# Kernel optimization log

Hardware: AMD Instinct MI355X
Metric: run time of the kernel (lower is better)

## Reference

```python
import jax, jax.numpy as jnp
import numpy as np
import math

B, S, D, H = 2, 2048, 1024, 16
DK = D // H


def setup_inputs() -> dict:
    key = jax.random.key(0)
    ks = jax.random.split(key, 12)
    s = 1.0 / math.sqrt(D)
    inp = {
        "query": jax.random.normal(ks[0], (B, S, D), jnp.float32),
        "key": jax.random.normal(ks[1], (B, S, D), jnp.float32),
        "value": jax.random.normal(ks[2], (B, S, D), jnp.float32),
        # causal mask, 0 = masked
        "mask": jnp.tril(jnp.ones((S, S), jnp.int32))[None].repeat(B, axis=0),
        "Wq": jax.random.normal(ks[3], (D, D), jnp.float32) * s,
        "bq": jnp.zeros((D,), jnp.float32),
        "Wk": jax.random.normal(ks[4], (D, D), jnp.float32) * s,
        "bk": jnp.zeros((D,), jnp.float32),
        "Wv": jax.random.normal(ks[5], (D, D), jnp.float32) * s,
        "bv": jnp.zeros((D,), jnp.float32),
        "Wo": jax.random.normal(ks[6], (D, D), jnp.float32) * s,
        "bo": jnp.zeros((D,), jnp.float32),
    }
    return inp


def _split_heads(x):
    # [B, S, D] -> [B, H, S, DK]
    b, s, _ = x.shape
    return x.reshape(b, s, H, DK).transpose(0, 2, 1, 3)


def reference(query, key, value, mask, Wq, bq, Wk, bk, Wv, bv, Wo, bo):
    q = _split_heads(query @ Wq + bq)
    k = _split_heads(key @ Wk + bk)
    v = _split_heads(value @ Wv + bv)
    scores = jnp.einsum("bhqd,bhkd->bhqk", q, k) / math.sqrt(DK)
    # mask: [B, Sq, Sk] -> broadcast over heads; 0 entries get -1e9
    scores = jnp.where(mask[:, None, :, :] == 0, jnp.float32(-1e9), scores)
    p = jax.nn.softmax(scores, axis=-1)  # dropout p=0 (eval) -> identity
    x = jnp.einsum("bhqk,bhkd->bhqd", p, v)
    x = x.transpose(0, 2, 1, 3).reshape(query.shape[0], -1, D)
    return x @ Wo + bo
```

## Files before the change

### kernel.cpp

```cpp
#include <hip/hip_runtime.h>
#include <hip/hip_bf16.h>
#include <stdint.h>


constexpr int BATCH = 2, SEQ = 2048, DIM = 1024, NH = 16, HD = 64;
constexpr int MROWS = BATCH * SEQ;

typedef __attribute__((ext_vector_type(4))) float f32x4;
typedef __attribute__((ext_vector_type(8))) short bf16x8;
typedef __attribute__((ext_vector_type(4))) int i32x4;

#define DEVI __device__ __forceinline__

DEVI ushort f2bf(float f) {
  __hip_bfloat16 h = __float2bfloat16(f);
  return __builtin_bit_cast(ushort, h);
}

DEVI f32x4 mfma16(bf16x8 a, bf16x8 b, f32x4 c) {
  return __builtin_amdgcn_mfma_f32_16x16x32_bf16(a, b, c, 0, 0, 0);
}

#if __has_builtin(__builtin_amdgcn_exp2f)
DEVI float fexp2(float x) { return __builtin_amdgcn_exp2f(x); }
#else
DEVI float fexp2(float x) { return exp2f(x); }
#endif

DEVI void gload16(const ushort* g, ushort* l) {
  __builtin_amdgcn_global_load_lds((const __attribute__((address_space(1))) void*)g,
                                   (__attribute__((address_space(3))) void*)l,
                                   16, 0, 0);
}

DEVI i32x4 cvt8(f32x4 a, f32x4 b) {
  union { ushort u[8]; i32x4 v; } r;
  #pragma unroll
  for (int j = 0; j < 4; ++j) r.u[j] = f2bf(a[j]);
  #pragma unroll
  for (int j = 0; j < 4; ++j) r.u[4 + j] = f2bf(b[j]);
  return r.v;
}

__global__ __launch_bounds__(256) void tw(const float* __restrict__ w0,
                                          const float* __restrict__ w1,
                                          const float* __restrict__ w2,
                                          const float* __restrict__ w3,
                                          ushort* __restrict__ t0,
                                          ushort* __restrict__ t1,
                                          ushort* __restrict__ t2,
                                          ushort* __restrict__ t3) {
  const float* W = blockIdx.z == 0 ? w0 : blockIdx.z == 1 ? w1 : blockIdx.z == 2 ? w2 : w3;
  ushort* T = blockIdx.z == 0 ? t0 : blockIdx.z == 1 ? t1 : blockIdx.z == 2 ? t2 : t3;
  __shared__ float tile[32][33];
  int k0 = blockIdx.x * 32, n0 = blockIdx.y * 32;
  int tx = threadIdx.x & 31, ty = threadIdx.x >> 5;
  #pragma unroll
  for (int i = 0; i < 32; i += 8) tile[ty + i][tx] = W[(size_t)(k0 + ty + i) * DIM + n0 + tx];
  __syncthreads();
  #pragma unroll
  for (int i = 0; i < 32; i += 8) T[(size_t)(n0 + ty + i) * DIM + k0 + tx] = f2bf(tile[tx][ty + i]);
}

struct GemmPtrs {
  const void* A[3];
  const ushort* Bt[3];
  const float* bias[3];
  void* C[3];
  float scale[3];
};

template <bool F32OUT, bool VT, bool AF32>
__global__ __launch_bounds__(256, 3) void gemm_bt(GemmPtrs gp, int M, int N, int K) {
  const int z = blockIdx.z;
  const float* __restrict__ A32 = (const float*)gp.A[z];
  const ushort* __restrict__ A16 = (const ushort*)gp.A[z];
  const ushort* __restrict__ Bt = gp.Bt[z];
  const float* __restrict__ bias = gp.bias[z];
  const float scale = gp.scale[z];
  const bool vsw = VT && (z == 2);

  __shared__ __align__(16) ushort As[2][128 * 32];
  __shared__ __align__(16) ushort Bs[2][128 * 32];

  const int tid = threadIdx.x;
  const int lane = tid & 63, wv = tid >> 6;
  const int wm = wv >> 1, wn = wv & 1;
  const int l15 = lane & 15, lg = lane >> 4;

  const int flat = blockIdx.y * 8 + blockIdx.x;
  const int xcd = flat & 7;
  const int j = flat >> 3;
  const int mslice = (int)gridDim.y >> 3;
  const int mpan = xcd * mslice + (j >> 3);
  const int npan = j & 7;
  const int m0 = mpan * 128, n0 = npan * 128;

  f32x4 acc[4][4];
  #pragma unroll
  for (int i = 0; i < 4; ++i)
    #pragma unroll
    for (int j2 = 0; j2 < 4; ++j2) acc[i][j2] = f32x4{0.f, 0.f, 0.f, 0.f};

  const int ci0 = tid, ci1 = tid + 256;
  const int ar0 = m0 + (ci0 >> 2), ar1 = m0 + (ci1 >> 2);
  const int ak0 = (ci0 & 3) * 8, ak1 = (ci1 & 3) * 8;
  const ushort* Ab0 = A16 + (size_t)ar0 * K + ak0;
  const ushort* Ab1 = A16 + (size_t)ar1 * K + ak1;
  const float* Af0 = A32 + (size_t)ar0 * K + ak0;
  const float* Af1 = A32 + (size_t)ar1 * K + ak1;
  const ushort* Bb0 = Bt + (size_t)(n0 + (ci0 >> 2)) * K + ak0;
  const ushort* Bb1 = Bt + (size_t)(n0 + (ci1 >> 2)) * K + ak1;

  f32x4 sA0, sA1, sA2, sA3;

  const int nk = K >> 5;
  if (AF32) {
    sA0 = *(const f32x4*)(Af0);     sA1 = *(const f32x4*)(Af0 + 4);
    sA2 = *(const f32x4*)(Af1);     sA3 = *(const f32x4*)(Af1 + 4);
    *(i32x4*)&As[0][ci0 * 8] = cvt8(sA0, sA1);
    *(i32x4*)&As[0][ci1 * 8] = cvt8(sA2, sA3);
    gload16(Bb0, &Bs[0][ci0 * 8]);
    gload16(Bb1, &Bs[0][ci1 * 8]);
    sA0 = *(const f32x4*)(Af0 + 32); sA1 = *(const f32x4*)(Af0 + 36);
    sA2 = *(const f32x4*)(Af1 + 32); sA3 = *(const f32x4*)(Af1 + 36);
  } else {
    gload16(Ab0, &As[0][ci0 * 8]);
    gload16(Ab1, &As[0][ci1 * 8]);
    gload16(Bb0, &Bs[0][ci0 * 8]);
    gload16(Bb1, &Bs[0][ci1 * 8]);
  }

  for (int kt = 0; kt < nk; ++kt) {
    const int cur = kt & 1;
    if (kt + 1 < nk) {
      const int ko = (kt + 1) << 5;
      if (!AF32) {
        gload16(Ab0 + ko, &As[cur ^ 1][ci0 * 8]);
        gload16(Ab1 + ko, &As[cur ^ 1][ci1 * 8]);
      }
      gload16(Bb0 + ko, &Bs[cur ^ 1][ci0 * 8]);
      gload16(Bb1 + ko, &Bs[cur ^ 1][ci1 * 8]);
      if (AF32)
        asm volatile("s_waitcnt vmcnt(6)" ::: "memory");
      else
        asm volatile("s_waitcnt vmcnt(4)" ::: "memory");
    } else {
      asm volatile("s_waitcnt vmcnt(0)" ::: "memory");
    }
    __builtin_amdgcn_s_barrier();
    __builtin_amdgcn_sched_barrier(0);

    const ushort* Afr = vsw ? &Bs[cur][0] : &As[cur][0];
    const ushort* Bfr = vsw ? &As[cur][0] : &Bs[cur][0];
    bf16x8 af[4], bfr[4];
    #pragma unroll
    for (int i = 0; i < 4; ++i) af[i] = *(const bf16x8*)&Afr[(wm * 64 + i * 16 + l15) * 32 + lg * 8];
    #pragma unroll
    for (int i = 0; i < 4; ++i) bfr[i] = *(const bf16x8*)&Bfr[(wn * 64 + i * 16 + l15) * 32 + lg * 8];
    #pragma unroll
    for (int i = 0; i < 4; ++i)
      #pragma unroll
      for (int j2 = 0; j2 < 4; ++j2) acc[i][j2] = mfma16(af[i], bfr[j2], acc[i][j2]);

    if (AF32 && kt + 1 < nk) {
      *(i32x4*)&As[cur ^ 1][ci0 * 8] = cvt8(sA0, sA1);
      *(i32x4*)&As[cur ^ 1][ci1 * 8] = cvt8(sA2, sA3);
      if (kt + 2 < nk) {
        const int ko2 = (kt + 2) << 5;
        sA0 = *(const f32x4*)(Af0 + ko2); sA1 = *(const f32x4*)(Af0 + ko2 + 4);
        sA2 = *(const f32x4*)(Af1 + ko2); sA3 = *(const f32x4*)(Af1 + ko2 + 4);
      }
      __builtin_amdgcn_sched_barrier(0);
      asm volatile("s_waitcnt lgkmcnt(0)" ::: "memory");
    }
    __builtin_amdgcn_s_barrier();
  }

  if (vsw) {
    ushort* Vt = (ushort*)gp.C[z];
    #pragma unroll
    for (int i = 0; i < 4; ++i)
      #pragma unroll
      for (int r = 0; r < 4; ++r) {
        int ch = n0 + wm * 64 + i * 16 + lg * 4 + r;
        float bch = bias[ch];
        int hh = ch >> 6, dch = ch & 63;
        #pragma unroll
        for (int j2 = 0; j2 < 4; ++j2) {
          int tok = m0 + wn * 64 + j2 * 16 + l15;
          int bb = tok >> 11, s = tok & 2047;
          float val = (acc[i][j2][r] + bch) * scale;
          Vt[(((size_t)bb * 16 + hh) * 64 + dch) * 2048 + s] = f2bf(val);
        }
      }
  } else {
    float bv[4];
    #pragma unroll
    for (int j2 = 0; j2 < 4; ++j2) bv[j2] = bias[n0 + wn * 64 + j2 * 16 + l15];
    #pragma unroll
    for (int i = 0; i < 4; ++i)
      #pragma unroll
      for (int j2 = 0; j2 < 4; ++j2)
        #pragma unroll
        for (int r = 0; r < 4; ++r) {
          int row = m0 + wm * 64 + i * 16 + lg * 4 + r;
          int col = n0 + wn * 64 + j2 * 16 + l15;
          float val = (acc[i][j2][r] + bv[j2]) * scale;
          if (F32OUT)
            ((float*)gp.C[z])[(size_t)row * N + col] = val;
          else
            ((ushort*)gp.C[z])[(size_t)row * N + col] = f2bf(val);
        }
  }
}

__global__ __launch_bounds__(256, 3) void attn(const ushort* __restrict__ Qp,
                                               const ushort* __restrict__ Kp,
                                               const ushort* __restrict__ Vtg,
                                               ushort* __restrict__ Xb) {
  __shared__ __align__(16) ushort Kl[2][64 * 64];
  __shared__ __align__(16) ushort Vl[2][64 * 64];
  __shared__ __align__(16) ushort Pl[4][16 * 64];

  const int bh = blockIdx.x;
  const int qt = (int)gridDim.y - 1 - (int)blockIdx.y;
  const int b = bh >> 4, h = bh & 15;
  const int tid = threadIdx.x;
  const int wv = tid >> 6, lane = tid & 63;
  const int l15 = lane & 15, lg = lane >> 4;
  const int swz = (l15 & 7) << 4;

  const size_t base = ((size_t)b * SEQ) * DIM + (size_t)h * HD;
  const ushort* Vtb = Vtg + (size_t)bh * HD * SEQ;

  const int qrow = qt * 64 + wv * 16 + l15;

  const ushort* qp = Qp + base + (size_t)qrow * DIM + lg * 8;
  bf16x8 qa[2] = {*(const bf16x8*)qp, *(const bf16x8*)(qp + 32)};

  f32x4 o[4];
  #pragma unroll
  for (int i = 0; i < 4; ++i) o[i] = f32x4{0.f, 0.f, 0.f, 0.f};
  float l_run = 0.f;

  const int ntiles = qt + 1;

  const int srow0 = tid >> 3, sc8 = tid & 7;
  const int srow1 = srow0 + 32;
  const int soff0 = (srow0 * 128 + sc8 * 16) ^ ((srow0 & 7) << 4);
  const int soff1 = (srow1 * 128 + sc8 * 16) ^ ((srow1 & 7) << 4);
  const ushort* Kb = Kp + base;

  i32x4 rk0 = *(const i32x4*)(Kb + (size_t)srow0 * DIM + sc8 * 8);
  i32x4 rk1 = *(const i32x4*)(Kb + (size_t)srow1 * DIM + sc8 * 8);
  i32x4 rv0 = *(const i32x4*)(Vtb + (size_t)srow0 * SEQ + sc8 * 8);
  i32x4 rv1 = *(const i32x4*)(Vtb + (size_t)srow1 * SEQ + sc8 * 8);
  *(i32x4*)((char*)&Kl[0][0] + soff0) = rk0;
  *(i32x4*)((char*)&Kl[0][0] + soff1) = rk1;
  *(i32x4*)((char*)&Vl[0][0] + soff0) = rv0;
  *(i32x4*)((char*)&Vl[0][0] + soff1) = rv1;

  for (int t = 0; t < ntiles; ++t) {
    const int cur = t & 1;
    const int kv0 = t * 64;

    if (t + 1 < ntiles) {
      const ushort* Kn = Kb + (size_t)(kv0 + 64) * DIM;
      const ushort* Vn = Vtb + (size_t)(kv0 + 64);
      rk0 = *(const i32x4*)(Kn + (size_t)srow0 * DIM + sc8 * 8);
      rk1 = *(const i32x4*)(Kn + (size_t)srow1 * DIM + sc8 * 8);
      rv0 = *(const i32x4*)(Vn + (size_t)srow0 * SEQ + sc8 * 8);
      rv1 = *(const i32x4*)(Vn + (size_t)srow1 * SEQ + sc8 * 8);
    }
    __syncthreads();

    const char* KL = (const char*)&Kl[cur][0];
    const char* VL = (const char*)&Vl[cur][0];

    f32x4 sc[4];
    #pragma unroll
    for (int n = 0; n < 4; ++n) sc[n] = f32x4{0.f, 0.f, 0.f, 0.f};
    __builtin_amdgcn_s_setprio(1);
    #pragma unroll
    for (int n = 0; n < 4; ++n) {
      #pragma unroll
      for (int kc = 0; kc < 2; ++kc) {
        int off = ((16 * n + l15) * 128 + kc * 64 + lg * 16) ^ swz;
        bf16x8 kf = *(const bf16x8*)(KL + off);
        sc[n] = mfma16(kf, qa[kc], sc[n]);
      }
    }
    __builtin_amdgcn_s_setprio(0);

    if (t == ntiles - 1) {
      #pragma unroll
      for (int n = 0; n < 4; ++n) {
        int kb0 = kv0 + 16 * n + lg * 4;
        #pragma unroll
        for (int r = 0; r < 4; ++r)
          if (kb0 + r > qrow) sc[n][r] = -1e30f;
      }
    }

    float rsum = 0.f;
    #pragma unroll
    for (int n = 0; n < 4; ++n)
      #pragma unroll
      for (int r = 0; r < 4; ++r) {
        float p = fexp2(sc[n][r]);
        sc[n][r] = p;
        rsum += p;
      }
    l_run += rsum;

    ushort* pb = &Pl[wv][0];
    #pragma unroll
    for (int n = 0; n < 4; ++n) {
      ushort4 pk = {f2bf(sc[n][0]), f2bf(sc[n][1]), f2bf(sc[n][2]), f2bf(sc[n][3])};
      int off = (l15 * 128 + n * 32 + lg * 8) ^ swz;
      *(ushort4*)((char*)pb + off) = pk;
    }
    bf16x8 pa[2];
    #pragma unroll
    for (int kc = 0; kc < 2; ++kc) {
      int off = (l15 * 128 + kc * 64 + lg * 16) ^ swz;
      pa[kc] = *(const bf16x8*)((char*)pb + off);
    }

    __builtin_amdgcn_s_setprio(1);
    #pragma unroll
    for (int kc = 0; kc < 2; ++kc)
      #pragma unroll
      for (int nd = 0; nd < 4; ++nd) {
        int off = ((16 * nd + l15) * 128 + kc * 64 + lg * 16) ^ swz;
        bf16x8 vf = *(const bf16x8*)(VL + off);
        o[nd] = mfma16(vf, pa[kc], o[nd]);
      }
    __builtin_amdgcn_s_setprio(0);

    if (t + 1 < ntiles) {
      char* KLn = (char*)&Kl[cur ^ 1][0];
      char* VLn = (char*)&Vl[cur ^ 1][0];
      *(i32x4*)(KLn + soff0) = rk0;
      *(i32x4*)(KLn + soff1) = rk1;
      *(i32x4*)(VLn + soff0) = rv0;
      *(i32x4*)(VLn + soff1) = rv1;
    }
  }

  float s = l_run;
  s += __shfl_xor(s, 16);
  s += __shfl_xor(s, 32);
  const float inv = 1.0f / s;
  ushort* xp = Xb + base + (size_t)qrow * DIM;
  #pragma unroll
  for (int nd = 0; nd < 4; ++nd) {
    ushort4 xk = {f2bf(o[nd][0] * inv), f2bf(o[nd][1] * inv),
                  f2bf(o[nd][2] * inv), f2bf(o[nd][3] * inv)};
    *(ushort4*)(xp + nd * 16 + lg * 4) = xk;
  }
}

extern "C" void kernel_launch(void* const* d_in, const int* in_sizes, int n_in,
                              void* d_out, int out_size, void* d_ws, size_t ws_size,
                              hipStream_t stream) {
  const float* query = (const float*)d_in[0];
  const float* keyp  = (const float*)d_in[1];
  const float* value = (const float*)d_in[2];
  const float* Wq = (const float*)d_in[4];
  const float* bq = (const float*)d_in[5];
  const float* Wk = (const float*)d_in[6];
  const float* bk = (const float*)d_in[7];
  const float* Wv = (const float*)d_in[8];
  const float* bv = (const float*)d_in[9];
  const float* Wo = (const float*)d_in[10];
  const float* bo = (const float*)d_in[11];
  float* out = (float*)d_out;

  char* w = (char*)d_ws;
  const size_t MAT = (size_t)MROWS * DIM * sizeof(ushort);
  const size_t WMT = (size_t)DIM * DIM * sizeof(ushort);
  ushort* WqT = (ushort*)w; w += WMT;
  ushort* WkT = (ushort*)w; w += WMT;
  ushort* WvT = (ushort*)w; w += WMT;
  ushort* WoT = (ushort*)w; w += WMT;
  ushort* Qp  = (ushort*)w; w += MAT;
  ushort* Kp  = (ushort*)w; w += MAT;
  ushort* Vt  = (ushort*)w; w += MAT;
  ushort* Xb  = (ushort*)w; w += MAT;

  tw<<<dim3(32, 32, 4), 256, 0, stream>>>(Wq, Wk, Wv, Wo, WqT, WkT, WvT, WoT);

  GemmPtrs g1;
  g1.A[0] = query; g1.A[1] = keyp; g1.A[2] = value;
  g1.Bt[0] = WqT; g1.Bt[1] = WkT; g1.Bt[2] = WvT;
  g1.bias[0] = bq; g1.bias[1] = bk; g1.bias[2] = bv;
  g1.C[0] = Qp; g1.C[1] = Kp; g1.C[2] = Vt;
  g1.scale[0] = 0.125f * 1.4426950408889634f; g1.scale[1] = 1.f; g1.scale[2] = 1.f;
  gemm_bt<false, true, true><<<dim3(DIM / 128, MROWS / 128, 3), 256, 0, stream>>>(g1, MROWS, DIM, DIM);

  attn<<<dim3(BATCH * NH, SEQ / 64), 256, 0, stream>>>(Qp, Kp, Vt, Xb);

  GemmPtrs g2;
  g2.A[0] = Xb; g2.A[1] = Xb; g2.A[2] = Xb;
  g2.Bt[0] = WoT; g2.Bt[1] = WoT; g2.Bt[2] = WoT;
  g2.bias[0] = bo; g2.bias[1] = bo; g2.bias[2] = bo;
  g2.C[0] = out; g2.C[1] = out; g2.C[2] = out;
  g2.scale[0] = 1.f; g2.scale[1] = 1.f; g2.scale[2] = 1.f;
  gemm_bt<true, false, false><<<dim3(DIM / 128, MROWS / 128, 1), 256, 0, stream>>>(g2, MROWS, DIM, DIM);
}
```

Baseline: 104.2 us.

## Stage fp32 A tiles directly to LDS with swizzle, convert to bf16 at fragment load

```diff
diff --git a/kernel.cpp b/kernel.cpp
--- a/kernel.cpp
+++ b/kernel.cpp
@@ -27,14 +27,14 @@
 DEVI float fexp2(float x) { return exp2f(x); }
 #endif
 
-DEVI void gload16(const ushort* g, ushort* l) {
+DEVI void gload16(const void* g, void* l) {
   __builtin_amdgcn_global_load_lds((const __attribute__((address_space(1))) void*)g,
                                    (__attribute__((address_space(3))) void*)l,
                                    16, 0, 0);
 }
 
-DEVI i32x4 cvt8(f32x4 a, f32x4 b) {
-  union { ushort u[8]; i32x4 v; } r;
+DEVI bf16x8 cvt8bf(f32x4 a, f32x4 b) {
+  union { ushort u[8]; bf16x8 v; } r;
   #pragma unroll
   for (int j = 0; j < 4; ++j) r.u[j] = f2bf(a[j]);
   #pragma unroll
@@ -70,7 +70,7 @@
   float scale[3];
 };
 
-template <bool F32OUT, bool VT, bool AF32>
+template <bool F32OUT, bool VT, bool AF32L>
 __global__ __launch_bounds__(256, 3) void gemm_bt(GemmPtrs gp, int M, int N, int K) {
   const int z = blockIdx.z;
   const float* __restrict__ A32 = (const float*)gp.A[z];
@@ -80,8 +80,9 @@
   const float scale = gp.scale[z];
   const bool vsw = VT && (z == 2);
 
-  __shared__ __align__(16) ushort As[2][128 * 32];
-  __shared__ __align__(16) ushort Bs[2][128 * 32];
+  constexpr int ASZ = AF32L ? 16384 : 8192;
+  __shared__ __align__(16) char As[2][ASZ];
+  __shared__ __align__(16) char Bs[2][8192];
 
   const int tid = threadIdx.x;
   const int lane = tid & 63, wv = tid >> 6;
@@ -103,45 +104,54 @@
     for (int j2 = 0; j2 < 4; ++j2) acc[i][j2] = f32x4{0.f, 0.f, 0.f, 0.f};
 
   const int ci0 = tid, ci1 = tid + 256;
-  const int ar0 = m0 + (ci0 >> 2), ar1 = m0 + (ci1 >> 2);
-  const int ak0 = (ci0 & 3) * 8, ak1 = (ci1 & 3) * 8;
-  const ushort* Ab0 = A16 + (size_t)ar0 * K + ak0;
-  const ushort* Ab1 = A16 + (size_t)ar1 * K + ak1;
-  const float* Af0 = A32 + (size_t)ar0 * K + ak0;
-  const float* Af1 = A32 + (size_t)ar1 * K + ak1;
-  const ushort* Bb0 = Bt + (size_t)(n0 + (ci0 >> 2)) * K + ak0;
-  const ushort* Bb1 = Bt + (size_t)(n0 + (ci1 >> 2)) * K + ak1;
-
-  f32x4 sA0, sA1, sA2, sA3;
+  const ushort* Bb0 = Bt + (size_t)(n0 + (ci0 >> 2)) * K + (ci0 & 3) * 8;
+  const ushort* Bb1 = Bt + (size_t)(n0 + (ci1 >> 2)) * K + (ci1 & 3) * 8;
+
+  const float* Af0s; const float* Af1s; const float* Af2s; const float* Af3s;
+  const ushort* Ab0; const ushort* Ab1;
+  int D0, D1, D2, D3;
+  if (AF32L) {
+    D0 = (tid + 0) * 16;   D1 = (tid + 256) * 16;
+    D2 = (tid + 512) * 16; D3 = (tid + 768) * 16;
+    int L0 = D0 ^ (((D0 >> 7) & 7) << 4);
+    int L1 = D1 ^ (((D1 >> 7) & 7) << 4);
+    int L2 = D2 ^ (((D2 >> 7) & 7) << 4);
+    int L3 = D3 ^ (((D3 >> 7) & 7) << 4);
+    Af0s = A32 + (size_t)(m0 + (L0 >> 7)) * K + ((L0 & 127) >> 2);
+    Af1s = A32 + (size_t)(m0 + (L1 >> 7)) * K + ((L1 & 127) >> 2);
+    Af2s = A32 + (size_t)(m0 + (L2 >> 7)) * K + ((L2 & 127) >> 2);
+    Af3s = A32 + (size_t)(m0 + (L3 >> 7)) * K + ((L3 & 127) >> 2);
+    Ab0 = nullptr; Ab1 = nullptr;
+  } else {
+    Ab0 = A16 + (size_t)(m0 + (ci0 >> 2)) * K + (ci0 & 3) * 8;
+    Ab1 = A16 + (size_t)(m0 + (ci1 >> 2)) * K + (ci1 & 3) * 8;
+    Af0s = Af1s = Af2s = Af3s = nullptr;
+    D0 = ci0 * 16; D1 = ci1 * 16; D2 = D3 = 0;
+  }
+
+  auto STAGE = [&](int buf, int kt) {
+    const int kof = kt << 5;
+    if (AF32L) {
+      gload16(Af0s + kof, &As[buf][D0]);
+      gload16(Af1s + kof, &As[buf][D1]);
+      gload16(Af2s + kof, &As[buf][D2]);
+      gload16(Af3s + kof, &As[buf][D3]);
+    } else {
+      gload16(Ab0 + kof, &As[buf][D0]);
+      gload16(Ab1 + kof, &As[buf][D1]);
+    }
+    gload16(Bb0 + kof, &Bs[buf][ci0 * 16]);
+    gload16(Bb1 + kof, &Bs[buf][ci1 * 16]);
+  };
 
   const int nk = K >> 5;
-  if (AF32) {
-    sA0 = *(const f32x4*)(Af0);     sA1 = *(const f32x4*)(Af0 + 4);
-    sA2 = *(const f32x4*)(Af1);     sA3 = *(const f32x4*)(Af1 + 4);
-    *(i32x4*)&As[0][ci0 * 8] = cvt8(sA0, sA1);
-    *(i32x4*)&As[0][ci1 * 8] = cvt8(sA2, sA3);
-    gload16(Bb0, &Bs[0][ci0 * 8]);
-    gload16(Bb1, &Bs[0][ci1 * 8]);
-    sA0 = *(const f32x4*)(Af0 + 32); sA1 = *(const f32x4*)(Af0 + 36);
-    sA2 = *(const f32x4*)(Af1 + 32); sA3 = *(const f32x4*)(Af1 + 36);
-  } else {
-    gload16(Ab0, &As[0][ci0 * 8]);
-    gload16(Ab1, &As[0][ci1 * 8]);
-    gload16(Bb0, &Bs[0][ci0 * 8]);
-    gload16(Bb1, &Bs[0][ci1 * 8]);
-  }
+  STAGE(0, 0);
 
   for (int kt = 0; kt < nk; ++kt) {
     const int cur = kt & 1;
     if (kt + 1 < nk) {
-      const int ko = (kt + 1) << 5;
-      if (!AF32) {
-        gload16(Ab0 + ko, &As[cur ^ 1][ci0 * 8]);
-        gload16(Ab1 + ko, &As[cur ^ 1][ci1 * 8]);
-      }
-      gload16(Bb0 + ko, &Bs[cur ^ 1][ci0 * 8]);
-      gload16(Bb1 + ko, &Bs[cur ^ 1][ci1 * 8]);
-      if (AF32)
+      STAGE(cur ^ 1, kt + 1);
+      if (AF32L)
         asm volatile("s_waitcnt vmcnt(6)" ::: "memory");
       else
         asm volatile("s_waitcnt vmcnt(4)" ::: "memory");
@@ -151,29 +161,31 @@
     __builtin_amdgcn_s_barrier();
     __builtin_amdgcn_sched_barrier(0);
 
-    const ushort* Afr = vsw ? &Bs[cur][0] : &As[cur][0];
-    const ushort* Bfr = vsw ? &As[cur][0] : &Bs[cur][0];
-    bf16x8 af[4], bfr[4];
-    #pragma unroll
-    for (int i = 0; i < 4; ++i) af[i] = *(const bf16x8*)&Afr[(wm * 64 + i * 16 + l15) * 32 + lg * 8];
-    #pragma unroll
-    for (int i = 0; i < 4; ++i) bfr[i] = *(const bf16x8*)&Bfr[(wn * 64 + i * 16 + l15) * 32 + lg * 8];
+    bf16x8 asf[4], bsf[4];
+    #pragma unroll
+    for (int i = 0; i < 4; ++i) {
+      int Ra = (vsw ? wn : wm) * 64 + i * 16 + l15;
+      if (AF32L) {
+        int Lb = Ra * 128 + lg * 32;
+        int s = (Ra & 7) << 4;
+        f32x4 lo = *(const f32x4*)&As[cur][Lb ^ s];
+        f32x4 hi = *(const f32x4*)&As[cur][(Lb + 16) ^ s];
+        asf[i] = cvt8bf(lo, hi);
+      } else {
+        asf[i] = *(const bf16x8*)&As[cur][Ra * 64 + lg * 16];
+      }
+      int Rb = (vsw ? wm : wn) * 64 + i * 16 + l15;
+      bsf[i] = *(const bf16x8*)&Bs[cur][Rb * 64 + lg * 16];
+    }
     #pragma unroll
     for (int i = 0; i < 4; ++i)
       #pragma unroll
-      for (int j2 = 0; j2 < 4; ++j2) acc[i][j2] = mfma16(af[i], bfr[j2], acc[i][j2]);
-
-    if (AF32 && kt + 1 < nk) {
-      *(i32x4*)&As[cur ^ 1][ci0 * 8] = cvt8(sA0, sA1);
-      *(i32x4*)&As[cur ^ 1][ci1 * 8] = cvt8(sA2, sA3);
-      if (kt + 2 < nk) {
-        const int ko2 = (kt + 2) << 5;
-        sA0 = *(const f32x4*)(Af0 + ko2); sA1 = *(const f32x4*)(Af0 + ko2 + 4);
-        sA2 = *(const f32x4*)(Af1 + ko2); sA3 = *(const f32x4*)(Af1 + ko2 + 4);
-      }
-      __builtin_amdgcn_sched_barrier(0);
-      asm volatile("s_waitcnt lgkmcnt(0)" ::: "memory");
-    }
+      for (int j2 = 0; j2 < 4; ++j2) {
+        bf16x8 aop = vsw ? bsf[i] : asf[i];
+        bf16x8 bop = vsw ? asf[j2] : bsf[j2];
+        acc[i][j2] = mfma16(aop, bop, acc[i][j2]);
+      }
+
     __builtin_amdgcn_s_barrier();
   }
 
@@ -215,7 +227,7 @@
   }
 }
 
-__global__ __launch_bounds__(256, 3) void attn(const ushort* __restrict__ Qp,
+__global__ __launch_bounds__(256, 4) void attn(const ushort* __restrict__ Qp,
                                                const ushort* __restrict__ Kp,
                                                const ushort* __restrict__ Vtg,
                                                ushort* __restrict__ Xb) {
```

Result: slower. 108.3 us (+4.0%).
